# Performance work log

Hardware: AMD Instinct MI355X
Metric: run time of the kernel (lower is better)

## Reference

```python
import jax, jax.numpy as jnp
import numpy as np
import math

D_MODEL, N_HEADS, BATCH, SEQ = 1024, 16, 2, 2048
D_HEAD = D_MODEL // N_HEADS


def setup_inputs() -> dict:
    key = jax.random.key(0)
    ks = jax.random.split(key, 5)
    w = lambda k: jax.random.normal(k, (D_MODEL, D_MODEL), jnp.float32) * 0.02
    return {
        "X": jax.random.normal(ks[0], (BATCH, SEQ, D_MODEL), jnp.float32),
        "W_q": w(ks[1]),
        "W_k": w(ks[2]),
        "W_v": w(ks[3]),
        "W_o": w(ks[4]),
        "g_q": jnp.ones((D_MODEL,), jnp.float32),
        "b_q": jnp.zeros((D_MODEL,), jnp.float32),
        "g_k": jnp.ones((D_MODEL,), jnp.float32),
        "b_k": jnp.zeros((D_MODEL,), jnp.float32),
        "cache_k": jnp.zeros((BATCH, N_HEADS, SEQ, D_HEAD), jnp.float32),
        "cache_v": jnp.zeros((BATCH, N_HEADS, SEQ, D_HEAD), jnp.float32),
        "start_pos": 0,
    }


def _layernorm(x, g, b, eps=1e-5):
    mu = jnp.mean(x, axis=-1, keepdims=True)
    xc = x - mu
    var = jnp.mean(xc * xc, axis=-1, keepdims=True)
    return xc * jax.lax.rsqrt(var + eps) * g + b


def reference(X, W_q, W_k, W_v, W_o, g_q, b_q, g_k, b_k, cache_k, cache_v, start_pos):
    batch, N, d_model = X.shape
    H = cache_k.shape[1]
    dh = d_model // H

    # QK-normed projections (torch Linear: x @ W^T)
    XQ = _layernorm(X @ W_q.T, g_q, b_q)
    XK = _layernorm(X @ W_k.T, g_k, b_k)
    XV = X @ W_v.T
    split = lambda t: t.reshape(batch, N, H, dh).transpose(0, 2, 1, 3)  # [b,h,n,d]
    XQ, XK, XV = split(XQ), split(XK), split(XV)

    # KV-cache scatter update, then slice to valid prefix (start_pos is static)
    cache_k = jax.lax.dynamic_update_slice(cache_k, XK, (0, 0, start_pos, 0))
    cache_v = jax.lax.dynamic_update_slice(cache_v, XV, (0, 0, start_pos, 0))
    M = start_pos + N
    K = cache_k[:, :, :M]
    V = cache_v[:, :, :M]

    logits = jnp.einsum('bhnd,bhmd->bhnm', XQ, K) / math.sqrt(dh)  # [b,h,N,M]

    # causal mask on the freshly written block [start_pos:M]
    tril = jnp.tril(jnp.ones((N, N), bool))
    full_mask = jnp.concatenate([jnp.ones((N, start_pos), bool), tril], axis=1)  # [N,M]
    logits = jnp.where(full_mask[None, None], logits, -jnp.inf)

    # selective forget-mask bias built from relu'd head-0 logits
    S = jax.nn.relu(logits[:, 0])               # relu(-inf) -> 0, matches torch
    S = S.at[..., 0].set(0.0)                   # zero first column
    S = S * (1.0 - jnp.eye(N, dtype=S.dtype))   # zero diagonal (valid since start_pos==0)
    S = jnp.roll(S, 1, axis=-2)                 # shift rows down by one
    S = S.at[..., 0, :].set(0.0)
    F_mask = jnp.cumsum(S, axis=-2)             # [b,N,M]

    logits = logits - F_mask[:, None]
    attn = jax.nn.softmax(logits, axis=-1)
    O = jnp.einsum('bhnm,bhmd->bhnd', attn, V)
    O = O.transpose(0, 2, 1, 3).reshape(batch, N, d_model)
    return O @ W_o.T
```

## Files before the change

### kernel.cpp

```cpp
#include <hip/hip_runtime.h>
#include <cstdint>
#include <cstddef>


typedef unsigned short u16;
typedef __attribute__((ext_vector_type(8))) __bf16 bf16x8;
typedef __attribute__((ext_vector_type(4))) float f32x4;

#define D_MODEL 1024
#define N_HEADS 16
#define BATCH   2
#define SEQ     2048
#define D_HEAD  64
#define ROWS    (BATCH*SEQ)
#define NSEG    16
#define SEGLEN  128
#define LOG2E   1.44269504f

static __device__ __forceinline__ u16 f2bf(float f){
  union { float f; uint32_t u; } v; v.f = f;
  uint32_t r = v.u + 0x7fffu + ((v.u >> 16) & 1u);
  return (u16)(r >> 16);
}
static __device__ __forceinline__ float bf2f(u16 h){
  union { uint32_t u; float f; } v; v.u = ((uint32_t)h) << 16;
  return v.f;
}
static __device__ __forceinline__ uint32_t pack2(float a, float b){
  uint32_t ua = __float_as_uint(a) + 0x8000u;
  uint32_t ub = __float_as_uint(b) + 0x8000u;
  return (ua >> 16) | (ub & 0xffff0000u);
}

__global__ void k_cast_all(const float* __restrict__ X,
                           u16* __restrict__ Xhi, u16* __restrict__ Xlo,
                           const float* __restrict__ Wq,
                           u16* __restrict__ Wqh, u16* __restrict__ Wql,
                           const float* __restrict__ Wk,
                           u16* __restrict__ Wkh, u16* __restrict__ Wkl,
                           const float* __restrict__ Wv, u16* __restrict__ Wvb,
                           const float* __restrict__ Wo, u16* __restrict__ Wob){
  int i = blockIdx.x*256 + threadIdx.x;
  if (i < 1572864){
    const float* src; u16 *dh, *dl; int base;
    if (i < 1048576){ src = X;  dh = Xhi; dl = Xlo; base = i; }
    else if (i < 1310720){ src = Wq; dh = Wqh; dl = Wql; base = i - 1048576; }
    else { src = Wk; dh = Wkh; dl = Wkl; base = i - 1310720; }
    float4 v = reinterpret_cast<const float4*>(src)[base];
    float vs[4] = {v.x, v.y, v.z, v.w};
    union { u16 s[4]; uint2 u; } uh, ul;
#pragma unroll
    for (int r=0;r<4;++r){
      uh.s[r] = f2bf(vs[r]);
      ul.s[r] = f2bf(vs[r] - bf2f(uh.s[r]));
    }
    reinterpret_cast<uint2*>(dh)[base] = uh.u;
    reinterpret_cast<uint2*>(dl)[base] = ul.u;
  } else {
    const float* src; u16* dst; int base;
    if (i < 1835008){ src = Wv; dst = Wvb; base = i - 1572864; }
    else { src = Wo; dst = Wob; base = i - 1835008; }
    float4 v = reinterpret_cast<const float4*>(src)[base];
    float vs[4] = {v.x, v.y, v.z, v.w};
    union { u16 s[4]; uint2 u; } uh;
#pragma unroll
    for (int r=0;r<4;++r) uh.s[r] = f2bf(vs[r]);
    reinterpret_cast<uint2*>(dst)[base] = uh.u;
  }
}

__global__ __launch_bounds__(256) void k_mega(
    const u16* __restrict__ Xhi, const u16* __restrict__ Xlo,
    const u16* __restrict__ Wh,  const u16* __restrict__ Wl,
    const u16* __restrict__ Wvb,
    float* __restrict__ C, float* __restrict__ Dlt, u16* __restrict__ Vt)
{
  __shared__ __align__(16) u16 smem[64*136];
  const int bid = blockIdx.x;
  const int tid = threadIdx.x, wv = tid>>6, ln = tid&63;
  const int lane15 = ln&15, quad = ln>>4;
  const int wm = wv&1, wn = wv>>1;
  const int sRow = ln>>2, sCol = (ln&3)*8;
  f32x4 z = {0.f,0.f,0.f,0.f};

  if (bid < 512){
    u16* As = smem;
    u16* Bs = smem + 4096;
    const size_t rowBase = (size_t)(bid>>4)*128, colBase = (size_t)(bid&15)*128;
    f32x4 acc[4][4];
#pragma unroll
    for (int i=0;i<4;++i)
#pragma unroll
      for (int j=0;j<4;++j) acc[i][j] = z;
    for (int kt = 0; kt < 32; ++kt) {
      __syncthreads();
#pragma unroll
      for (int c = 0; c < 2; ++c) {
        int chunk = wv*2 + c;
        int r = chunk*16 + sRow;
        const u16* ga = Xhi + (rowBase + r)*1024 + kt*32 + sCol;
        const u16* gb = Wh  + (colBase + r)*1024 + kt*32 + sCol;
        __builtin_amdgcn_global_load_lds(
            (const __attribute__((address_space(1))) void*)ga,
            (__attribute__((address_space(3))) void*)(As + chunk*512), 16, 0, 0);
        __builtin_amdgcn_global_load_lds(
            (const __attribute__((address_space(1))) void*)gb,
            (__attribute__((address_space(3))) void*)(Bs + chunk*512), 16, 0, 0);
      }
      __syncthreads();
      bf16x8 af[4], bfb[4];
#pragma unroll
      for (int t=0;t<4;++t){
        af[t]  = *reinterpret_cast<const bf16x8*>(As + (wm*64 + t*16 + lane15)*32 + quad*8);
        bfb[t] = *reinterpret_cast<const bf16x8*>(Bs + (wn*64 + t*16 + lane15)*32 + quad*8);
      }
#pragma unroll
      for (int i=0;i<4;++i)
#pragma unroll
        for (int j=0;j<4;++j)
          acc[i][j] = __builtin_amdgcn_mfma_f32_16x16x32_bf16(af[i], bfb[j], acc[i][j], 0,0,0);
    }
#pragma unroll
    for (int i=0;i<4;++i){
      size_t row = rowBase + wm*64 + i*16 + quad*4;
#pragma unroll
      for (int j=0;j<4;++j){
        size_t col = colBase + wn*64 + j*16 + lane15;
#pragma unroll
        for (int r=0;r<4;++r)
          C[(row+r)*2048 + col] = acc[i][j][r];
      }
    }
  } else if (bid < 640){
    u16* As = smem;
    u16* Bs = smem + 4096;
    const int idx = bid - 512;
    const int cx = idx & 1;
    const int cy = (idx >> 1) & 31;
    const int cz = idx >> 6;
    const size_t rowBase = (size_t)cy*128;
    const size_t wbase = cx ? (size_t)1024*1024 : 0;
    const u16* Ap = cz ? Xlo : Xhi;
    const u16* Bp = (cz ? Wh : Wl) + wbase;
    f32x4 acc[4][2];
#pragma unroll
    for (int i=0;i<4;++i){ acc[i][0] = z; acc[i][1] = z; }
    for (int kt = 0; kt < 32; ++kt) {
      __syncthreads();
#pragma unroll
      for (int c = 0; c < 2; ++c) {
        int chunk = wv*2 + c;
        int r = chunk*16 + sRow;
        const u16* ga = Ap + (rowBase + r)*1024 + kt*32 + sCol;
        __builtin_amdgcn_global_load_lds(
            (const __attribute__((address_space(1))) void*)ga,
            (__attribute__((address_space(3))) void*)(As + chunk*512), 16, 0, 0);
      }
      {
        int r = wv*16 + sRow;
        const u16* gb = Bp + (size_t)r*1024 + kt*32 + sCol;
        __builtin_amdgcn_global_load_lds(
            (const __attribute__((address_space(1))) void*)gb,
            (__attribute__((address_space(3))) void*)(Bs + wv*512), 16, 0, 0);
      }
      __syncthreads();
      bf16x8 af[4], bfb[2];
#pragma unroll
      for (int t=0;t<4;++t)
        af[t]  = *reinterpret_cast<const bf16x8*>(As + (wm*64 + t*16 + lane15)*32 + quad*8);
#pragma unroll
      for (int t=0;t<2;++t)
        bfb[t] = *reinterpret_cast<const bf16x8*>(Bs + (wn*32 + t*16 + lane15)*32 + quad*8);
#pragma unroll
      for (int i=0;i<4;++i)
#pragma unroll
        for (int j=0;j<2;++j)
          acc[i][j] = __builtin_amdgcn_mfma_f32_16x16x32_bf16(af[i], bfb[j], acc[i][j], 0,0,0);
    }
#pragma unroll
    for (int i=0;i<4;++i){
      size_t row = rowBase + wm*64 + i*16 + quad*4;
#pragma unroll
      for (int j=0;j<2;++j){
        size_t col = (size_t)cx*64 + wn*32 + j*16 + lane15;
#pragma unroll
        for (int r=0;r<4;++r)
          atomicAdd(&Dlt[(row+r)*128 + col], acc[i][j][r]);
      }
    }
  } else {
    u16* As = smem;
    u16* Bs = smem + 4096;
    const int idx = bid - 640;
    const int bx = idx & 15, by = idx >> 4;
    const size_t rowBase = (size_t)by*128, colBase = (size_t)bx*64;
    f32x4 acc[4][2];
#pragma unroll
    for (int i=0;i<4;++i){ acc[i][0] = z; acc[i][1] = z; }
    for (int kt = 0; kt < 32; ++kt) {
      __syncthreads();
#pragma unroll
      for (int c = 0; c < 2; ++c) {
        int chunk = wv*2 + c;
        int r = chunk*16 + sRow;
        const u16* ga = Xhi + (rowBase + r)*1024 + kt*32 + sCol;
        __builtin_amdgcn_global_load_lds(
            (const __attribute__((address_space(1))) void*)ga,
            (__attribute__((address_space(3))) void*)(As + chunk*512), 16, 0, 0);
      }
      {
        int r = wv*16 + sRow;
        const u16* gb = Wvb + (colBase + r)*1024 + kt*32 + sCol;
        __builtin_amdgcn_global_load_lds(
            (const __attribute__((address_space(1))) void*)gb,
            (__attribute__((address_space(3))) void*)(Bs + wv*512), 16, 0, 0);
      }
      __syncthreads();
      bf16x8 af[4], bfb[2];
#pragma unroll
      for (int t=0;t<4;++t)
        af[t]  = *reinterpret_cast<const bf16x8*>(As + (wm*64 + t*16 + lane15)*32 + quad*8);
#pragma unroll
      for (int t=0;t<2;++t)
        bfb[t] = *reinterpret_cast<const bf16x8*>(Bs + (wn*32 + t*16 + lane15)*32 + quad*8);
#pragma unroll
      for (int i=0;i<4;++i)
#pragma unroll
        for (int j=0;j<2;++j)
          acc[i][j] = __builtin_amdgcn_mfma_f32_16x16x32_bf16(af[i], bfb[j], acc[i][j], 0,0,0);
    }
    __syncthreads();
#pragma unroll
    for (int i=0;i<4;++i){
      int nl = wm*64 + i*16 + quad*4;
#pragma unroll
      for (int j=0;j<2;++j){
        int dl = wn*32 + j*16 + lane15;
#pragma unroll
        for (int r=0;r<4;++r)
          smem[dl*136 + nl + r] = f2bf(acc[i][j][r]);
      }
    }
    __syncthreads();
    const int b = by >> 4;
    const int n0 = (by & 15) * 128;
    const int bh = b*N_HEADS + bx;
    const int d = tid >> 2, seg = tid & 3;
    u16* dst = Vt + ((size_t)(bh*64 + d))*SEQ + n0 + seg*32;
    const u16* srcl = smem + d*136 + seg*32;
#pragma unroll
    for (int k=0;k<4;++k)
      *reinterpret_cast<uint4*>(dst + k*8) = *reinterpret_cast<const uint4*>(srcl + k*8);
  }
}

__global__ __launch_bounds__(256) void k_ln_pack2(
    const float* __restrict__ C, const float* __restrict__ Dlt,
    const float* __restrict__ gq, const float* __restrict__ bq,
    const float* __restrict__ gk, const float* __restrict__ bk,
    u16* __restrict__ Qh, u16* __restrict__ Kh,
    u16* __restrict__ Q0l, u16* __restrict__ K0l)
{
  const int row = blockIdx.x;
  const int tid = threadIdx.x;
  const float* cr = C + (size_t)row*2048;
  float4 vq = reinterpret_cast<const float4*>(cr)[tid];
  float4 vk = reinterpret_cast<const float4*>(cr)[256 + tid];
  const int h = tid >> 4;
  if (h == 0){
    float4 dq = reinterpret_cast<const float4*>(Dlt + (size_t)row*128)[tid&15];
    vq.x+=dq.x; vq.y+=dq.y; vq.z+=dq.z; vq.w+=dq.w;
  }
  if (h == 0){
    float4 dk = reinterpret_cast<const float4*>(Dlt + (size_t)row*128 + 64)[tid&15];
    vk.x+=dk.x; vk.y+=dk.y; vk.z+=dk.z; vk.w+=dk.w;
  }
  float sq  = vq.x+vq.y+vq.z+vq.w;
  float s2q = vq.x*vq.x+vq.y*vq.y+vq.z*vq.z+vq.w*vq.w;
  float sk  = vk.x+vk.y+vk.z+vk.w;
  float s2k = vk.x*vk.x+vk.y*vk.y+vk.z*vk.z+vk.w*vk.w;
#pragma unroll
  for (int o=32;o;o>>=1){
    sq += __shfl_xor(sq,o);  s2q += __shfl_xor(s2q,o);
    sk += __shfl_xor(sk,o);  s2k += __shfl_xor(s2k,o);
  }
  __shared__ float red[4][4];
  if ((tid&63)==0){
    red[tid>>6][0]=sq; red[tid>>6][1]=s2q; red[tid>>6][2]=sk; red[tid>>6][3]=s2k;
  }
  __syncthreads();
  sq  = red[0][0]+red[1][0]+red[2][0]+red[3][0];
  s2q = red[0][1]+red[1][1]+red[2][1]+red[3][1];
  sk  = red[0][2]+red[1][2]+red[2][2]+red[3][2];
  s2k = red[0][3]+red[1][3]+red[2][3]+red[3][3];
  const float muq = sq*(1.f/D_MODEL);
  const float rsq = rsqrtf(s2q*(1.f/D_MODEL) - muq*muq + 1e-5f);
  const float muk = sk*(1.f/D_MODEL);
  const float rsk = rsqrtf(s2k*(1.f/D_MODEL) - muk*muk + 1e-5f);
  const int b = row >> 11, n = row & (SEQ-1);
  const int d0 = (tid & 15)*4;
  float4 gqv = reinterpret_cast<const float4*>(gq)[tid];
  float4 bqv = reinterpret_cast<const float4*>(bq)[tid];
  float4 gkv = reinterpret_cast<const float4*>(gk)[tid];
  float4 bkv = reinterpret_cast<const float4*>(bk)[tid];
  float xq[4] = {vq.x,vq.y,vq.z,vq.w}, xk[4] = {vk.x,vk.y,vk.z,vk.w};
  float gQ[4] = {gqv.x,gqv.y,gqv.z,gqv.w}, bQ[4] = {bqv.x,bqv.y,bqv.z,bqv.w};
  float gK[4] = {gkv.x,gkv.y,gkv.z,gkv.w}, bK[4] = {bkv.x,bkv.y,bkv.z,bkv.w};
  union { u16 s[4]; uint2 u; } qh, ql, kh, kl;
#pragma unroll
  for (int r=0;r<4;++r){
    float yq = (xq[r]-muq)*rsq*gQ[r] + bQ[r];
    qh.s[r] = f2bf(yq);
    ql.s[r] = f2bf(yq - bf2f(qh.s[r]));
    float yk = (xk[r]-muk)*rsk*gK[r] + bK[r];
    kh.s[r] = f2bf(yk);
    kl.s[r] = f2bf(yk - bf2f(kh.s[r]));
  }
  size_t dst = (((size_t)(b*N_HEADS + h))*SEQ + n)*D_HEAD + d0;
  *reinterpret_cast<uint2*>(Qh + dst) = qh.u;
  *reinterpret_cast<uint2*>(Kh + dst) = kh.u;
  if (h == 0){
    size_t dl = ((size_t)b*SEQ + n)*D_HEAD + d0;
    *reinterpret_cast<uint2*>(Q0l + dl) = ql.u;
    *reinterpret_cast<uint2*>(K0l + dl) = kl.u;
  }
}

__global__ __launch_bounds__(256) void k_s0(
    const u16* Qh, const u16* Q0l, const u16* Kh, const u16* K0l,
    float* __restrict__ S0, float* __restrict__ seg)
{
  const int b = blockIdx.z;
  const int bm = blockIdx.y;
  const int bn = blockIdx.x;
  const int tid = threadIdx.x;
  if (bn > bm){
    if (tid < 128) seg[((size_t)b*NSEG + bm)*SEQ + bn*128 + tid] = 0.f;
    return;
  }
  float* Sb = S0 + (size_t)b*SEQ*SEQ;
  __shared__ __align__(16) u16 As[128*32];
  __shared__ __align__(16) u16 Bs[128*32];
  __shared__ float cs[2][128];
  const int wv = tid>>6, ln = tid&63;
  const int lane15 = ln&15, quad = ln>>4;
  const int wm = wv&1, wn = wv>>1;
  f32x4 acc[4][4];
  f32x4 z = {0.f,0.f,0.f,0.f};
#pragma unroll
  for (int i=0;i<4;++i)
#pragma unroll
    for (int j=0;j<4;++j) acc[i][j] = z;
  const u16* Qb  = Qh  + (size_t)b*N_HEADS*SEQ*D_HEAD;
  const u16* Kb  = Kh  + (size_t)b*N_HEADS*SEQ*D_HEAD;
  const u16* Qlb = Q0l + (size_t)b*SEQ*D_HEAD;
  const u16* Klb = K0l + (size_t)b*SEQ*D_HEAD;
  const u16* Aps[3] = {Qb, Qb, Qlb};
  const u16* Bps[3] = {Kb, Klb, Kb};
  const int sRow = ln>>2, sCol = (ln&3)*8;
  const size_t rowBase = (size_t)bm*128, colBase = (size_t)bn*128;
  for (int p = 0; p < 3; ++p) {
    const u16* Ap = Aps[p];
    const u16* Bp = Bps[p];
    for (int kt = 0; kt < 2; ++kt) {
      __syncthreads();
#pragma unroll
      for (int c = 0; c < 2; ++c) {
        int chunk = wv*2 + c;
        int r = chunk*16 + sRow;
        const u16* ga = Ap + (rowBase + r)*D_HEAD + kt*32 + sCol;
        const u16* gb = Bp + (colBase + r)*D_HEAD + kt*32 + sCol;
        __builtin_amdgcn_global_load_lds(
            (const __attribute__((address_space(1))) void*)ga,
            (__attribute__((address_space(3))) void*)(As + chunk*512), 16, 0, 0);
        __builtin_amdgcn_global_load_lds(
            (const __attribute__((address_space(1))) void*)gb,
            (__attribute__((address_space(3))) void*)(Bs + chunk*512), 16, 0, 0);
      }
      __syncthreads();
      bf16x8 af[4], bfb[4];
#pragma unroll
      for (int t=0;t<4;++t){
        af[t]  = *reinterpret_cast<const bf16x8*>(As + (wm*64 + t*16 + lane15)*32 + quad*8);
        bfb[t] = *reinterpret_cast<const bf16x8*>(Bs + (wn*64 + t*16 + lane15)*32 + quad*8);
      }
#pragma unroll
      for (int i=0;i<4;++i)
#pragma unroll
        for (int j=0;j<4;++j)
          acc[i][j] = __builtin_amdgcn_mfma_f32_16x16x32_bf16(af[i], bfb[j], acc[i][j], 0,0,0);
    }
  }
  float csum[4] = {0.f,0.f,0.f,0.f};
#pragma unroll
  for (int i=0;i<4;++i){
#pragma unroll
    for (int j=0;j<4;++j){
#pragma unroll
      for (int r=0;r<4;++r){
        int jg = (int)rowBase + wm*64 + i*16 + quad*4 + r;
        int mg = (int)colBase + wn*64 + j*16 + lane15;
        float l = acc[i][j][r]*0.125f;
        float s = (mg >= 1 && mg < jg) ? fmaxf(l, 0.f) : 0.f;
        Sb[(size_t)jg*SEQ + mg] = s;
        csum[j] += s;
      }
    }
  }
#pragma unroll
  for (int j=0;j<4;++j){
    float v = csum[j];
    v += __shfl_xor(v, 16);
    v += __shfl_xor(v, 32);
    if (ln < 16) cs[wm][wn*64 + j*16 + ln] = v;
  }
  __syncthreads();
  if (tid < 128)
    seg[((size_t)b*NSEG + bm)*SEQ + bn*128 + tid] = cs[0][tid] + cs[1][tid];
}

__global__ void k_seg_apply(float* __restrict__ SF, const float* __restrict__ seg){
  int m = blockIdx.x*256 + threadIdx.x;
  int s = blockIdx.y, b = blockIdx.z;
  const float* sb = seg + (size_t)b*NSEG*SEQ;
  float run = 0.f;
  for (int t=0; t<s; ++t) run += sb[(size_t)t*SEQ + m];
  float* Sb = SF + (size_t)b*SEQ*SEQ;
  const int j0 = s*SEGLEN;
  for (int i=0;i<SEGLEN;++i){
    size_t idx = (size_t)(j0 + i)*SEQ + m;
    float t = Sb[idx];
    Sb[idx] = -run*LOG2E;
    run += (j0 + i > m) ? t : 0.f;
  }
}

__global__ __launch_bounds__(256, 2) void k_attn(
    const u16* __restrict__ Qh, const u16* __restrict__ Kh,
    const u16* __restrict__ Vt, const float* __restrict__ F,
    u16* __restrict__ Ob)
{
  __shared__ __align__(16) u16 Ks[2][64*64];
  __shared__ __align__(16) u16 Vs[2][64*64];
  const int h = blockIdx.x, b = blockIdx.z;
  const int nt = b ? (int)(gridDim.y - 1 - blockIdx.y) : (int)blockIdx.y;
  const int tid = threadIdx.x, wv = tid>>6, ln = tid&63;
  const int lane15 = ln&15, quad = ln>>4;
  const u16* Qbh = Qh + ((size_t)(b*N_HEADS + h))*SEQ*D_HEAD;
  const u16* Kbh = Kh + ((size_t)(b*N_HEADS + h))*SEQ*D_HEAD;
  const u16* Vbh = Vt + ((size_t)(b*N_HEADS + h))*D_HEAD*SEQ;
  const float* Fb = F + (size_t)b*SEQ*SEQ;
  const int n0 = nt*128;
  const int swz = (ln&7) ^ ((ln>>3)&7);
  const int fswz = lane15 & 7;
  const int srow = ln>>3;
  const int nchunks = 2*nt + 2;

  bf16x8 qf[2][2];
#pragma unroll
  for (int ns=0; ns<2; ++ns)
#pragma unroll
    for (int kt=0; kt<2; ++kt){
      int n = n0 + wv*32 + ns*16 + lane15;
      qf[ns][kt] = *reinterpret_cast<const bf16x8*>(Qbh + (size_t)n*D_HEAD + kt*32 + quad*8);
    }

  f32x4 z = {0.f,0.f,0.f,0.f};
  float psum[2] = {0.f, 0.f};
  f32x4 acc_o[2][4];
#pragma unroll
  for (int ns=0;ns<2;++ns)
#pragma unroll
    for (int no=0;no<4;++no) acc_o[ns][no] = z;

  auto stage = [&](int mc, int buf){
#pragma unroll
    for (int c=0;c<2;++c){
      int chunk = wv*2 + c;
      int r = chunk*8 + srow;
      const u16* gk = Kbh + (size_t)(mc*64 + r)*D_HEAD + swz*8;
      const u16* gv = Vbh + (size_t)r*SEQ + mc*64 + swz*8;
      __builtin_amdgcn_global_load_lds(
          (const __attribute__((address_space(1))) void*)gk,
          (__attribute__((address_space(3))) void*)(&Ks[buf][chunk*512]), 16, 0, 0);
      __builtin_amdgcn_global_load_lds(
          (const __attribute__((address_space(1))) void*)gv,
          (__attribute__((address_space(3))) void*)(&Vs[buf][chunk*512]), 16, 0, 0);
    }
  };
  stage(0, 0);
  const float c1 = 0.125f*LOG2E;

  for (int mc = 0; mc < nchunks; ++mc) {
    const int cur = mc & 1;
    __syncthreads();
    if (mc+1 < nchunks) stage(mc+1, 1-cur);
    const bool diag = (mc >= 2*nt);
#pragma unroll
    for (int ns=0; ns<2; ++ns){
      const int n_loc = wv*32 + ns*16 + lane15;
      const int n_g = n0 + n_loc;
      const float* Fr = Fb + (size_t)n_g*SEQ + mc*64;
      f32x4 accs[4];
#pragma unroll
      for (int ms=0;ms<4;++ms) accs[ms] = z;
#pragma unroll
      for (int kt=0; kt<2; ++kt){
#pragma unroll
        for (int ms=0; ms<4; ++ms){
          bf16x8 a = *reinterpret_cast<const bf16x8*>(
              &Ks[cur][(ms*16 + lane15)*64 + (((kt*4 + quad) ^ fswz) * 8)]);
          accs[ms] = __builtin_amdgcn_mfma_f32_16x16x32_bf16(a, qf[ns][kt], accs[ms], 0,0,0);
        }
      }
      uint32_t pw[4][2];
#pragma unroll
      for (int ms=0; ms<4; ++ms){
        f32x4 fv = *reinterpret_cast<const f32x4*>(Fr + ms*16 + quad*4);
        f32x4 t = accs[ms];
        float p[4];
#pragma unroll
        for (int r=0;r<4;++r){
          float l2 = fmaf(t[r], c1, fv[r]);
          if (diag){
            int m_g = mc*64 + ms*16 + quad*4 + r;
            l2 = (m_g > n_g) ? -1e30f : l2;
          }
          p[r] = __builtin_amdgcn_exp2f(l2);
        }
        psum[ns] += (p[0]+p[1]) + (p[2]+p[3]);
        pw[ms][0] = pack2(p[0], p[1]);
        pw[ms][1] = pack2(p[2], p[3]);
      }
#pragma unroll
      for (int kt=0; kt<2; ++kt){
        union { uint32_t u[4]; bf16x8 v; } pa;
#pragma unroll
        for (int w=0; w<4; ++w){
          int sl = lane15 + 16*((quad&1)*2 + (w>>1));
          uint32_t t0 = (uint32_t)__shfl((int)pw[2*kt  ][w&1], sl);
          uint32_t t1 = (uint32_t)__shfl((int)pw[2*kt+1][w&1], sl);
          pa.u[w] = (quad < 2) ? t0 : t1;
        }
#pragma unroll
        for (int no=0; no<4; ++no){
          int d = no*16 + lane15;
          bf16x8 vb = *reinterpret_cast<const bf16x8*>(
              &Vs[cur][d*64 + (((kt*4 + quad) ^ (d&7)) * 8)]);
          acc_o[ns][no] = __builtin_amdgcn_mfma_f32_16x16x32_bf16(pa.v, vb, acc_o[ns][no], 0,0,0);
        }
      }
    }
  }
#pragma unroll
  for (int ns=0; ns<2; ++ns){
    float s = psum[ns];
    s += __shfl_xor(s, 16);
    s += __shfl_xor(s, 32);
    f32x4 inv;
#pragma unroll
    for (int r=0;r<4;++r)
      inv[r] = __builtin_amdgcn_rcpf(__shfl(s, quad*4 + r));
#pragma unroll
    for (int no=0; no<4; ++no){
#pragma unroll
      for (int r=0;r<4;++r){
        float o = acc_o[ns][no][r] * inv[r];
        int row = n0 + wv*32 + ns*16 + quad*4 + r;
        Ob[((size_t)(b*SEQ + row))*D_MODEL + h*64 + no*16 + lane15] = f2bf(o);
      }
    }
  }
}

__global__ __launch_bounds__(256) void k_gemm_nt64(
    const u16* __restrict__ A0, const u16* __restrict__ B0,
    float* __restrict__ C, int N, int K)
{
  __shared__ __align__(16) u16 As[128*32];
  __shared__ __align__(16) u16 Bs[64*32];
  const int tid = threadIdx.x, wv = tid>>6, ln = tid&63;
  const int lane15 = ln&15, quad = ln>>4;
  const int wm = wv&1, wn = wv>>1;
  const size_t rowBase = (size_t)blockIdx.y*128, colBase = (size_t)blockIdx.x*64;
  f32x4 acc[4][2];
  f32x4 z = {0.f,0.f,0.f,0.f};
#pragma unroll
  for (int i=0;i<4;++i){ acc[i][0] = z; acc[i][1] = z; }
  const int ktiles = K >> 5;
  const int sRow = ln>>2, sCol = (ln&3)*8;
  for (int kt = 0; kt < ktiles; ++kt) {
    __syncthreads();
#pragma unroll
    for (int c = 0; c < 2; ++c) {
      int chunk = wv*2 + c;
      int r = chunk*16 + sRow;
      const u16* ga = A0 + (rowBase + r)*K + kt*32 + sCol;
      __builtin_amdgcn_global_load_lds(
          (const __attribute__((address_space(1))) void*)ga,
          (__attribute__((address_space(3))) void*)(As + chunk*512), 16, 0, 0);
    }
    {
      int r = wv*16 + sRow;
      const u16* gb = B0 + (colBase + r)*K + kt*32 + sCol;
      __builtin_amdgcn_global_load_lds(
          (const __attribute__((address_space(1))) void*)gb,
          (__attribute__((address_space(3))) void*)(Bs + wv*512), 16, 0, 0);
    }
    __syncthreads();
    bf16x8 af[4], bfb[2];
#pragma unroll
    for (int t=0;t<4;++t)
      af[t]  = *reinterpret_cast<const bf16x8*>(As + (wm*64 + t*16 + lane15)*32 + quad*8);
#pragma unroll
    for (int t=0;t<2;++t)
      bfb[t] = *reinterpret_cast<const bf16x8*>(Bs + (wn*32 + t*16 + lane15)*32 + quad*8);
#pragma unroll
    for (int i=0;i<4;++i)
#pragma unroll
      for (int j=0;j<2;++j)
        acc[i][j] = __builtin_amdgcn_mfma_f32_16x16x32_bf16(af[i], bfb[j], acc[i][j], 0,0,0);
  }
#pragma unroll
  for (int i=0;i<4;++i){
    size_t row = rowBase + wm*64 + i*16 + quad*4;
#pragma unroll
    for (int j=0;j<2;++j){
      size_t col = colBase + wn*32 + j*16 + lane15;
#pragma unroll
      for (int r=0;r<4;++r)
        C[(row+r)*N + col] = acc[i][j][r];
    }
  }
}

extern "C" void kernel_launch(void* const* d_in, const int* in_sizes, int n_in,
                              void* d_out, int out_size, void* d_ws, size_t ws_size,
                              hipStream_t stream)
{
  (void)in_sizes; (void)n_in; (void)out_size; (void)ws_size;
  const float* X  = (const float*)d_in[0];
  const float* Wq = (const float*)d_in[1];
  const float* Wk = (const float*)d_in[2];
  const float* Wv = (const float*)d_in[3];
  const float* Wo = (const float*)d_in[4];
  const float* gq = (const float*)d_in[5];
  const float* bq = (const float*)d_in[6];
  const float* gk = (const float*)d_in[7];
  const float* bk = (const float*)d_in[8];
  float* out = (float*)d_out;

  char* ws = (char*)d_ws;
  size_t off = 0;
  auto alloc = [&](size_t bytes)->char*{
    char* p = ws + off; off += (bytes + 255) & ~(size_t)255; return p;
  };
  u16* Xhi  = (u16*)alloc((size_t)ROWS*D_MODEL*2);
  u16* Xlo  = (u16*)alloc((size_t)ROWS*D_MODEL*2);
  u16* Wqkh = (u16*)alloc((size_t)2*D_MODEL*D_MODEL*2);
  u16* Wqkl = (u16*)alloc((size_t)2*D_MODEL*D_MODEL*2);
  u16* Wvb  = (u16*)alloc((size_t)D_MODEL*D_MODEL*2);
  u16* Wob  = (u16*)alloc((size_t)D_MODEL*D_MODEL*2);
  u16* Qhp  = (u16*)alloc((size_t)BATCH*N_HEADS*SEQ*D_HEAD*2);
  u16* Khp  = (u16*)alloc((size_t)BATCH*N_HEADS*SEQ*D_HEAD*2);
  u16* Q0l  = (u16*)alloc((size_t)BATCH*SEQ*D_HEAD*2);
  u16* K0l  = (u16*)alloc((size_t)BATCH*SEQ*D_HEAD*2);
  u16* Vtp  = (u16*)alloc((size_t)BATCH*N_HEADS*D_HEAD*SEQ*2);
  u16* Obf  = (u16*)alloc((size_t)ROWS*D_MODEL*2);
  float* Dlt = (float*)alloc((size_t)ROWS*128*4);
  float* Seg = (float*)alloc((size_t)BATCH*NSEG*SEQ*4);
  float* SF  = (float*)alloc((size_t)BATCH*SEQ*SEQ*4);
  float* C32 = SF;

  hipMemsetAsync(Dlt, 0, (size_t)ROWS*128*4, stream);

  k_cast_all<<<8192, 256, 0, stream>>>(
      X, Xhi, Xlo,
      Wq, Wqkh, Wqkl,
      Wk, Wqkh + (size_t)D_MODEL*D_MODEL, Wqkl + (size_t)D_MODEL*D_MODEL,
      Wv, Wvb, Wo, Wob);

  k_mega<<<1152, 256, 0, stream>>>(Xhi, Xlo, Wqkh, Wqkl, Wvb, C32, Dlt, Vtp);

  k_ln_pack2<<<ROWS, 256, 0, stream>>>(C32, Dlt, gq, bq, gk, bk, Qhp, Khp, Q0l, K0l);
  k_s0<<<dim3(16, 16, BATCH), 256, 0, stream>>>(Qhp, Q0l, Khp, K0l, SF, Seg);
  k_seg_apply<<<dim3(8, NSEG, BATCH), 256, 0, stream>>>(SF, Seg);
  k_attn<<<dim3(N_HEADS, SEQ/128, BATCH), 256, 0, stream>>>(Qhp, Khp, Vtp, SF, Obf);
  k_gemm_nt64<<<dim3(16, 32), 256, 0, stream>>>(Obf, Wob, out, D_MODEL, D_MODEL);
}
```

Measured before the change: 334.1 us.

## Shrink attention query tile to 64 rows and split forget-mask cumsum into finer segments

The attention kernel now handles 64 query rows per block, one 16-row slice per wave, instead of 128. This doubles the grid, raises the occupancy hint to 4 blocks per CU and hoists the forget-mask loads ahead of the QK MFMAs. The segmented cumsum uses 64 segments of 32 rows instead of 16 of 128, so the serial column scan in k_seg_apply is shorter and has more parallel blocks; k_s0 now writes four partial column sums per tile. In exchange, K/V tiles are reused across fewer query rows, so the attention kernel issues more global traffic, and k_seg_apply's prefix loop over earlier segments gets longer.

```diff
diff --git a/kernel.cpp b/kernel.cpp
--- a/kernel.cpp
+++ b/kernel.cpp
@@ -13,8 +13,8 @@
 #define SEQ     2048
 #define D_HEAD  64
 #define ROWS    (BATCH*SEQ)
-#define NSEG    16
-#define SEGLEN  128
+#define NSEG    64
+#define SEGLEN  32
 #define LOG2E   1.44269504f
 
 static __device__ __forceinline__ u16 f2bf(float f){
@@ -270,8 +270,6 @@
   if (h == 0){
     float4 dq = reinterpret_cast<const float4*>(Dlt + (size_t)row*128)[tid&15];
     vq.x+=dq.x; vq.y+=dq.y; vq.z+=dq.z; vq.w+=dq.w;
-  }
-  if (h == 0){
     float4 dk = reinterpret_cast<const float4*>(Dlt + (size_t)row*128 + 64)[tid&15];
     vk.x+=dk.x; vk.y+=dk.y; vk.z+=dk.z; vk.w+=dk.w;
   }
@@ -335,13 +333,14 @@
   const int bn = blockIdx.x;
   const int tid = threadIdx.x;
   if (bn > bm){
-    if (tid < 128) seg[((size_t)b*NSEG + bm)*SEQ + bn*128 + tid] = 0.f;
+    for (int t = tid; t < 512; t += 256)
+      seg[((size_t)b*NSEG + bm*4 + (t>>7))*SEQ + bn*128 + (t&127)] = 0.f;
     return;
   }
   float* Sb = S0 + (size_t)b*SEQ*SEQ;
   __shared__ __align__(16) u16 As[128*32];
   __shared__ __align__(16) u16 Bs[128*32];
-  __shared__ float cs[2][128];
+  __shared__ float cs[4][128];
   const int wv = tid>>6, ln = tid&63;
   const int lane15 = ln&15, quad = ln>>4;
   const int wm = wv&1, wn = wv>>1;
@@ -391,7 +390,7 @@
           acc[i][j] = __builtin_amdgcn_mfma_f32_16x16x32_bf16(af[i], bfb[j], acc[i][j], 0,0,0);
     }
   }
-  float csum[4] = {0.f,0.f,0.f,0.f};
+  float csum[2][4] = {{0.f,0.f,0.f,0.f},{0.f,0.f,0.f,0.f}};
 #pragma unroll
   for (int i=0;i<4;++i){
 #pragma unroll
@@ -403,20 +402,23 @@
         float l = acc[i][j][r]*0.125f;
         float s = (mg >= 1 && mg < jg) ? fmaxf(l, 0.f) : 0.f;
         Sb[(size_t)jg*SEQ + mg] = s;
-        csum[j] += s;
-      }
-    }
-  }
-#pragma unroll
-  for (int j=0;j<4;++j){
-    float v = csum[j];
-    v += __shfl_xor(v, 16);
-    v += __shfl_xor(v, 32);
-    if (ln < 16) cs[wm][wn*64 + j*16 + ln] = v;
+        csum[i>>1][j] += s;
+      }
+    }
+  }
+#pragma unroll
+  for (int h2=0;h2<2;++h2){
+#pragma unroll
+    for (int j=0;j<4;++j){
+      float v = csum[h2][j];
+      v += __shfl_xor(v, 16);
+      v += __shfl_xor(v, 32);
+      if (ln < 16) cs[wm*2 + h2][wn*64 + j*16 + ln] = v;
+    }
   }
   __syncthreads();
-  if (tid < 128)
-    seg[((size_t)b*NSEG + bm)*SEQ + bn*128 + tid] = cs[0][tid] + cs[1][tid];
+  for (int t = tid; t < 512; t += 256)
+    seg[((size_t)b*NSEG + bm*4 + (t>>7))*SEQ + bn*128 + (t&127)] = cs[t>>7][t&127];
 }
 
 __global__ void k_seg_apply(float* __restrict__ SF, const float* __restrict__ seg){
@@ -427,6 +429,7 @@
   for (int t=0; t<s; ++t) run += sb[(size_t)t*SEQ + m];
   float* Sb = SF + (size_t)b*SEQ*SEQ;
   const int j0 = s*SEGLEN;
+#pragma unroll 8
   for (int i=0;i<SEGLEN;++i){
     size_t idx = (size_t)(j0 + i)*SEQ + m;
     float t = Sb[idx];
@@ -435,7 +438,7 @@
   }
 }
 
-__global__ __launch_bounds__(256, 2) void k_attn(
+__global__ __launch_bounds__(256, 4) void k_attn(
     const u16* __restrict__ Qh, const u16* __restrict__ Kh,
     const u16* __restrict__ Vt, const float* __restrict__ F,
     u16* __restrict__ Ob)
@@ -450,36 +453,30 @@
   const u16* Kbh = Kh + ((size_t)(b*N_HEADS + h))*SEQ*D_HEAD;
   const u16* Vbh = Vt + ((size_t)(b*N_HEADS + h))*D_HEAD*SEQ;
   const float* Fb = F + (size_t)b*SEQ*SEQ;
-  const int n0 = nt*128;
+  const int n_loc = wv*16 + lane15;
+  const int n_g = nt*64 + n_loc;
   const int swz = (ln&7) ^ ((ln>>3)&7);
   const int fswz = lane15 & 7;
   const int srow = ln>>3;
-  const int nchunks = 2*nt + 2;
-
-  bf16x8 qf[2][2];
-#pragma unroll
-  for (int ns=0; ns<2; ++ns)
-#pragma unroll
-    for (int kt=0; kt<2; ++kt){
-      int n = n0 + wv*32 + ns*16 + lane15;
-      qf[ns][kt] = *reinterpret_cast<const bf16x8*>(Qbh + (size_t)n*D_HEAD + kt*32 + quad*8);
-    }
+
+  bf16x8 qf[2];
+#pragma unroll
+  for (int kt=0; kt<2; ++kt)
+    qf[kt] = *reinterpret_cast<const bf16x8*>(Qbh + (size_t)n_g*D_HEAD + kt*32 + quad*8);
 
   f32x4 z = {0.f,0.f,0.f,0.f};
-  float psum[2] = {0.f, 0.f};
-  f32x4 acc_o[2][4];
-#pragma unroll
-  for (int ns=0;ns<2;++ns)
-#pragma unroll
-    for (int no=0;no<4;++no) acc_o[ns][no] = z;
-
-  auto stage = [&](int mc, int buf){
+  f32x4 psum = z;
+  f32x4 acc_o[4];
+#pragma unroll
+  for (int no=0;no<4;++no) acc_o[no] = z;
+
+  auto stage = [&](int mt, int buf){
 #pragma unroll
     for (int c=0;c<2;++c){
       int chunk = wv*2 + c;
       int r = chunk*8 + srow;
-      const u16* gk = Kbh + (size_t)(mc*64 + r)*D_HEAD + swz*8;
-      const u16* gv = Vbh + (size_t)r*SEQ + mc*64 + swz*8;
+      const u16* gk = Kbh + (size_t)(mt*64 + r)*D_HEAD + swz*8;
+      const u16* gv = Vbh + (size_t)r*SEQ + mt*64 + swz*8;
       __builtin_amdgcn_global_load_lds(
           (const __attribute__((address_space(1))) void*)gk,
           (__attribute__((address_space(3))) void*)(&Ks[buf][chunk*512]), 16, 0, 0);
@@ -491,84 +488,79 @@
   stage(0, 0);
   const float c1 = 0.125f*LOG2E;
 
-  for (int mc = 0; mc < nchunks; ++mc) {
-    const int cur = mc & 1;
+  for (int mt = 0; mt <= nt; ++mt) {
+    const int cur = mt & 1;
     __syncthreads();
-    if (mc+1 < nchunks) stage(mc+1, 1-cur);
-    const bool diag = (mc >= 2*nt);
-#pragma unroll
-    for (int ns=0; ns<2; ++ns){
-      const int n_loc = wv*32 + ns*16 + lane15;
-      const int n_g = n0 + n_loc;
-      const float* Fr = Fb + (size_t)n_g*SEQ + mc*64;
-      f32x4 accs[4];
-#pragma unroll
-      for (int ms=0;ms<4;++ms) accs[ms] = z;
-#pragma unroll
-      for (int kt=0; kt<2; ++kt){
-#pragma unroll
-        for (int ms=0; ms<4; ++ms){
-          bf16x8 a = *reinterpret_cast<const bf16x8*>(
-              &Ks[cur][(ms*16 + lane15)*64 + (((kt*4 + quad) ^ fswz) * 8)]);
-          accs[ms] = __builtin_amdgcn_mfma_f32_16x16x32_bf16(a, qf[ns][kt], accs[ms], 0,0,0);
+    if (mt < nt) stage(mt+1, 1-cur);
+    const float* Fr = Fb + (size_t)n_g*SEQ + mt*64;
+    f32x4 fv[4];
+#pragma unroll
+    for (int ms=0; ms<4; ++ms)
+      fv[ms] = *reinterpret_cast<const f32x4*>(Fr + ms*16 + quad*4);
+    f32x4 accs[4];
+#pragma unroll
+    for (int ms=0;ms<4;++ms) accs[ms] = z;
+#pragma unroll
+    for (int kt=0; kt<2; ++kt){
+#pragma unroll
+      for (int ms=0; ms<4; ++ms){
+        bf16x8 a = *reinterpret_cast<const bf16x8*>(
+            &Ks[cur][(ms*16 + lane15)*64 + (((kt*4 + quad) ^ fswz) * 8)]);
+        accs[ms] = __builtin_amdgcn_mfma_f32_16x16x32_bf16(a, qf[kt], accs[ms], 0,0,0);
+      }
+    }
+    const bool diag = (mt == nt);
+    uint32_t pw[4][2];
+#pragma unroll
+    for (int ms=0; ms<4; ++ms){
+      f32x4 t = accs[ms];
+      float p[4];
+#pragma unroll
+      for (int r=0;r<4;++r){
+        float l2 = fmaf(t[r], c1, fv[ms][r]);
+        if (diag){
+          int ml = ms*16 + quad*4 + r;
+          l2 = (ml > n_loc) ? -1e30f : l2;
         }
-      }
-      uint32_t pw[4][2];
-#pragma unroll
-      for (int ms=0; ms<4; ++ms){
-        f32x4 fv = *reinterpret_cast<const f32x4*>(Fr + ms*16 + quad*4);
-        f32x4 t = accs[ms];
-        float p[4];
-#pragma unroll
-        for (int r=0;r<4;++r){
-          float l2 = fmaf(t[r], c1, fv[r]);
-          if (diag){
-            int m_g = mc*64 + ms*16 + quad*4 + r;
-            l2 = (m_g > n_g) ? -1e30f : l2;
-          }
-          p[r] = __builtin_amdgcn_exp2f(l2);
-        }
-        psum[ns] += (p[0]+p[1]) + (p[2]+p[3]);
-        pw[ms][0] = pack2(p[0], p[1]);
-        pw[ms][1] = pack2(p[2], p[3]);
-      }
-#pragma unroll
-      for (int kt=0; kt<2; ++kt){
-        union { uint32_t u[4]; bf16x8 v; } pa;
-#pragma unroll
-        for (int w=0; w<4; ++w){
-          int sl = lane15 + 16*((quad&1)*2 + (w>>1));
-          uint32_t t0 = (uint32_t)__shfl((int)pw[2*kt  ][w&1], sl);
-          uint32_t t1 = (uint32_t)__shfl((int)pw[2*kt+1][w&1], sl);
-          pa.u[w] = (quad < 2) ? t0 : t1;
-        }
-#pragma unroll
-        for (int no=0; no<4; ++no){
-          int d = no*16 + lane15;
-          bf16x8 vb = *reinterpret_cast<const bf16x8*>(
-              &Vs[cur][d*64 + (((kt*4 + quad) ^ (d&7)) * 8)]);
-          acc_o[ns][no] = __builtin_amdgcn_mfma_f32_16x16x32_bf16(pa.v, vb, acc_o[ns][no], 0,0,0);
-        }
-      }
-    }
-  }
-#pragma unroll
-  for (int ns=0; ns<2; ++ns){
-    float s = psum[ns];
-    s += __shfl_xor(s, 16);
-    s += __shfl_xor(s, 32);
-    f32x4 inv;
-#pragma unroll
-    for (int r=0;r<4;++r)
-      inv[r] = __builtin_amdgcn_rcpf(__shfl(s, quad*4 + r));
-#pragma unroll
-    for (int no=0; no<4; ++no){
-#pragma unroll
-      for (int r=0;r<4;++r){
-        float o = acc_o[ns][no][r] * inv[r];
-        int row = n0 + wv*32 + ns*16 + quad*4 + r;
-        Ob[((size_t)(b*SEQ + row))*D_MODEL + h*64 + no*16 + lane15] = f2bf(o);
-      }
+        p[r] = __builtin_amdgcn_exp2f(l2);
+      }
+      psum[0]+=p[0]; psum[1]+=p[1]; psum[2]+=p[2]; psum[3]+=p[3];
+      pw[ms][0] = pack2(p[0], p[1]);
+      pw[ms][1] = pack2(p[2], p[3]);
+    }
+#pragma unroll
+    for (int kt=0; kt<2; ++kt){
+      union { uint32_t u[4]; bf16x8 v; } pa;
+#pragma unroll
+      for (int w=0; w<4; ++w){
+        int sl = lane15 + 16*((quad&1)*2 + (w>>1));
+        uint32_t t0 = (uint32_t)__shfl((int)pw[2*kt  ][w&1], sl);
+        uint32_t t1 = (uint32_t)__shfl((int)pw[2*kt+1][w&1], sl);
+        pa.u[w] = (quad < 2) ? t0 : t1;
+      }
+#pragma unroll
+      for (int no=0; no<4; ++no){
+        int d = no*16 + lane15;
+        bf16x8 vb = *reinterpret_cast<const bf16x8*>(
+            &Vs[cur][d*64 + (((kt*4 + quad) ^ (d&7)) * 8)]);
+        acc_o[no] = __builtin_amdgcn_mfma_f32_16x16x32_bf16(pa.v, vb, acc_o[no], 0,0,0);
+      }
+    }
+  }
+  float s = (psum[0]+psum[1]) + (psum[2]+psum[3]);
+  s += __shfl_xor(s, 16);
+  s += __shfl_xor(s, 32);
+  f32x4 inv;
+#pragma unroll
+  for (int r=0;r<4;++r)
+    inv[r] = __builtin_amdgcn_rcpf(__shfl(s, quad*4 + r));
+#pragma unroll
+  for (int no=0; no<4; ++no){
+#pragma unroll
+    for (int r=0;r<4;++r){
+      float o = acc_o[no][r] * inv[r];
+      int row = nt*64 + wv*16 + quad*4 + r;
+      Ob[((size_t)(b*SEQ + row))*D_MODEL + h*64 + no*16 + lane15] = f2bf(o);
     }
   }
 }
@@ -685,6 +677,6 @@
   k_ln_pack2<<<ROWS, 256, 0, stream>>>(C32, Dlt, gq, bq, gk, bk, Qhp, Khp, Q0l, K0l);
   k_s0<<<dim3(16, 16, BATCH), 256, 0, stream>>>(Qhp, Q0l, Khp, K0l, SF, Seg);
   k_seg_apply<<<dim3(8, NSEG, BATCH), 256, 0, stream>>>(SF, Seg);
-  k_attn<<<dim3(N_HEADS, SEQ/128, BATCH), 256, 0, stream>>>(Qhp, Khp, Vtp, SF, Obf);
+  k_attn<<<dim3(N_HEADS, SEQ/64, BATCH), 256, 0, stream>>>(Qhp, Khp, Vtp, SF, Obf);
   k_gemm_nt64<<<dim3(16, 32), 256, 0, stream>>>(Obf, Wob, out, D_MODEL, D_MODEL);
 }
```

Result: faster. 311.9 us (-6.6%).
